# Performance work log

Measured on AMD Instinct MI355X. Metric: run time of the kernel, lower is better.

The kernel has to match this reference:

```python
import jax, jax.numpy as jnp
import numpy as np

B, T, D, H = 8, 1024, 768, 12
HD = D // H          # 64 head dim
WINDOW = 768         # sliding-window width hardcoded in the block
EPS = 1e-5

def _layer_norm(x, w, b):
    mu = jnp.mean(x, axis=-1, keepdims=True)
    var = jnp.mean(jnp.square(x - mu), axis=-1, keepdims=True)
    return (x - mu) * jax.lax.rsqrt(var + EPS) * w + b

def setup_inputs() -> dict:
    key = jax.random.key(0)
    ks = jax.random.split(key, 16)
    s = 0.02
    return {
        "x": jax.random.normal(ks[0], (B, T, D), jnp.float32),
        "attn_mask": jnp.ones((B, T), jnp.int32),
        "ln1_w": jnp.ones((D,), jnp.float32),
        "ln1_b": jnp.zeros((D,), jnp.float32),
        "w_attn": jax.random.normal(ks[1], (D, 3 * D), jnp.float32) * s,
        "b_attn": jnp.zeros((3 * D,), jnp.float32),
        "w_proj": jax.random.normal(ks[2], (D, D), jnp.float32) * s,
        "b_proj": jnp.zeros((D,), jnp.float32),
        "ln2_w": jnp.ones((D,), jnp.float32),
        "ln2_b": jnp.zeros((D,), jnp.float32),
        "w_fc": jax.random.normal(ks[3], (D, 4 * D), jnp.float32) * s,
        "b_fc": jnp.zeros((4 * D,), jnp.float32),
        "w_fc_proj": jax.random.normal(ks[4], (4 * D, D), jnp.float32) * s,
        "b_fc_proj": jnp.zeros((D,), jnp.float32),
    }

def reference(x, attn_mask, ln1_w, ln1_b, w_attn, b_attn, w_proj, b_proj,
              ln2_w, ln2_b, w_fc, b_fc, w_fc_proj, b_fc_proj):
    dtype = x.dtype
    # --- attention sub-block ---
    x1 = _layer_norm(x, ln1_w, ln1_b)
    qkv = x1 @ w_attn + b_attn                       # [B,T,3D]
    q, k, v = jnp.split(qkv, 3, axis=-1)
    q = q.reshape(B, T, H, HD).transpose(0, 2, 1, 3)  # [B,H,T,HD]
    k = k.reshape(B, T, H, HD).transpose(0, 2, 1, 3)
    v = v.reshape(B, T, H, HD).transpose(0, 2, 1, 3)
    # causal + sliding-window + padding mask (additive bias, as in source)
    i = jnp.arange(T)[:, None]
    j = jnp.arange(T)[None, :]
    keep = (j <= i) & (j >= i - WINDOW + 1)           # [T,T]
    keep = keep[None, None] & (attn_mask.astype(bool))[:, None, None, :]  # [B,1,T,T]
    mask_bias = jnp.where(keep, jnp.zeros((), dtype), jnp.full((), jnp.finfo(dtype).min, dtype))
    scale = 1.0 / np.sqrt(HD)
    scores = jnp.einsum('bhqd,bhkd->bhqk', q, k) * scale + mask_bias
    probs = jax.nn.softmax(scores, axis=-1)
    attn = jnp.einsum('bhqk,bhkd->bhqd', probs, v)    # [B,H,T,HD]
    attn = attn.transpose(0, 2, 1, 3).reshape(B, T, D)
    a = attn @ w_proj + b_proj
    x = x + a
    # --- MLP sub-block ---
    x3 = _layer_norm(x, ln2_w, ln2_b)
    h = jax.nn.gelu(x3 @ w_fc + b_fc, approximate=False)
    m = h @ w_fc_proj + b_fc_proj
    return x + m
```

## Files before the change

### kernel.cpp

```cpp
#include <hip/hip_runtime.h>
#include <hip/hip_bf16.h>
#include <math.h>

#define NB 8
#define NT 1024
#define ND 768
#define NH 12
#define HD 64
#define WINDOW 768
#define LN_EPS 1e-5f
#define NEGF -3.4028234663852886e38f

static const int BT = NB * NT;

typedef __bf16 bf16x8 __attribute__((ext_vector_type(8)));
typedef float  f32x4  __attribute__((ext_vector_type(4)));
typedef unsigned short ushort_t;

__device__ __forceinline__ unsigned short f2bf(float f) {
    __hip_bfloat16 h = __float2bfloat16(f);
    return __builtin_bit_cast(unsigned short, h);
}

__device__ __forceinline__ void load_lds16(const void* g, void* l) {
    __builtin_amdgcn_global_load_lds((const __attribute__((address_space(1))) unsigned int*)g,
                                     (__attribute__((address_space(3))) unsigned int*)l,
                                     16, 0, 0);
}

__global__ __launch_bounds__(256) void transpose_bf16(const float* __restrict__ w,
                                                      ushort_t* __restrict__ wt,
                                                      int K, int N) {
    __shared__ float t[32][33];
    const int n0 = blockIdx.x * 32, k0 = blockIdx.y * 32;
    const int tx = threadIdx.x, ty = threadIdx.y;
    for (int r = ty; r < 32; r += 8)
        t[r][tx] = w[(size_t)(k0 + r) * N + n0 + tx];
    __syncthreads();
    for (int r = ty; r < 32; r += 8)
        wt[(size_t)(n0 + r) * K + k0 + tx] = f2bf(t[tx][r]);
}

__global__ __launch_bounds__(256) void transpose_v(const ushort_t* __restrict__ qkvb,
                                                   ushort_t* __restrict__ vT) {
    const int t0 = blockIdx.x * 64;
    const int h = blockIdx.y, b = blockIdx.z;
    __shared__ ushort_t sm[64 * 72];
    const int tid = threadIdx.x;
    #pragma unroll
    for (int p = 0; p < 2; p++) {
        int idx = p * 256 + tid;
        int r = idx >> 3, c = idx & 7;
        *(bf16x8*)&sm[r * 72 + c * 8] =
            *(const bf16x8*)(qkvb + (size_t)(b * NT + t0 + r) * (3 * ND) + 2 * ND + h * HD + c * 8);
    }
    __syncthreads();
    #pragma unroll
    for (int p = 0; p < 2; p++) {
        int idx = p * 256 + tid;
        int d = idx >> 3, c2 = idx & 7;
        ushort_t tmp[8];
        #pragma unroll
        for (int j = 0; j < 8; j++) tmp[j] = sm[(c2 * 8 + j) * 72 + d];
        *(bf16x8*)(vT + ((size_t)((b * NH + h) * HD + d)) * NT + t0 + c2 * 8) = *(bf16x8*)tmp;
    }
}

__global__ __launch_bounds__(256) void ln_kernel(const float* __restrict__ x,
                                                 const float* __restrict__ w,
                                                 const float* __restrict__ b,
                                                 ushort_t* __restrict__ out) {
    const int row  = blockIdx.x * 4 + (threadIdx.x >> 6);
    const int lane = threadIdx.x & 63;
    const float* xr = x + (size_t)row * ND;

    float4 v[3];
    #pragma unroll
    for (int s = 0; s < 3; s++) v[s] = *(const float4*)(xr + s * 256 + lane * 4);

    float sum = 0.f;
    #pragma unroll
    for (int s = 0; s < 3; s++) sum += v[s].x + v[s].y + v[s].z + v[s].w;
    #pragma unroll
    for (int off = 1; off < 64; off <<= 1) sum += __shfl_xor(sum, off, 64);
    const float mu = sum * (1.0f / ND);

    float var = 0.f;
    #pragma unroll
    for (int s = 0; s < 3; s++) {
        float a0 = v[s].x - mu, a1 = v[s].y - mu, a2 = v[s].z - mu, a3 = v[s].w - mu;
        var += a0 * a0 + a1 * a1 + a2 * a2 + a3 * a3;
    }
    #pragma unroll
    for (int off = 1; off < 64; off <<= 1) var += __shfl_xor(var, off, 64);
    const float rstd = rsqrtf(var * (1.0f / ND) + LN_EPS);

    #pragma unroll
    for (int s = 0; s < 3; s++) {
        const int col = s * 256 + lane * 4;
        float4 w4 = *(const float4*)(w + col);
        float4 b4 = *(const float4*)(b + col);
        ushort4 r;
        r.x = f2bf((v[s].x - mu) * rstd * w4.x + b4.x);
        r.y = f2bf((v[s].y - mu) * rstd * w4.y + b4.y);
        r.z = f2bf((v[s].z - mu) * rstd * w4.z + b4.z);
        r.w = f2bf((v[s].w - mu) * rstd * w4.w + b4.w);
        *(ushort4*)(out + (size_t)row * ND + col) = r;
    }
}

template <int EPI>
__global__ __launch_bounds__(256) void gemm_bt(const ushort_t* __restrict__ A,
                                               const ushort_t* __restrict__ Bt,
                                               const float* __restrict__ bias,
                                               const float* __restrict__ resid,
                                               void* __restrict__ Cout,
                                               int M, int N, int K) {
    __shared__ __align__(16) ushort_t smem[2][2][128 * 32];

    const int tid  = threadIdx.x;
    const int bm   = blockIdx.y * 128;
    const int bn   = blockIdx.x * 128;
    const int lane = tid & 63;
    const int wave = tid >> 6;
    const int wm   = (wave & 1) * 64;
    const int wn   = (wave >> 1) * 64;
    const int fcol = lane & 15;
    const int quad = lane >> 4;

    f32x4 acc[4][4] = {};

    const int srow = tid >> 2, scg = (tid & 3) * 8;

    auto issue = [&](int k0, int buf) {
        #pragma unroll
        for (int p = 0; p < 2; p++) {
            const int row = srow + p * 64;
            const int flat = (p * 256 + tid) * 8;
            load_lds16(A  + (size_t)(bm + row) * K + k0 + scg, &smem[buf][0][flat]);
            load_lds16(Bt + (size_t)(bn + row) * K + k0 + scg, &smem[buf][1][flat]);
        }
    };

    issue(0, 0);
    const int KT = K >> 5;
    for (int kt = 0; kt < KT; kt++) {
        const int cur = kt & 1;
        __syncthreads();
        if (kt + 1 < KT) issue((kt + 1) << 5, cur ^ 1);

        bf16x8 a[4], b[4];
        #pragma unroll
        for (int i = 0; i < 4; i++)
            a[i] = *(const bf16x8*)&smem[cur][0][(wm + i * 16 + fcol) * 32 + quad * 8];
        #pragma unroll
        for (int j = 0; j < 4; j++)
            b[j] = *(const bf16x8*)&smem[cur][1][(wn + j * 16 + fcol) * 32 + quad * 8];
        #pragma unroll
        for (int i = 0; i < 4; i++)
            #pragma unroll
            for (int j = 0; j < 4; j++)
                acc[i][j] = __builtin_amdgcn_mfma_f32_16x16x32_bf16(a[i], b[j], acc[i][j], 0, 0, 0);
    }

    if (EPI == 1) {
        #pragma unroll
        for (int j = 0; j < 4; j++) {
            const int gcol = bn + wn + j * 16 + fcol;
            const float bs = bias[gcol];
            #pragma unroll
            for (int i = 0; i < 4; i++) {
                #pragma unroll
                for (int r = 0; r < 4; r++) {
                    const int grow = bm + wm + i * 16 + quad * 4 + r;
                    float val = acc[i][j][r] + bs + resid[(size_t)grow * N + gcol];
                    ((float*)Cout)[(size_t)grow * N + gcol] = val;
                }
            }
        }
    } else {
        __syncthreads();
        ushort_t* Cs = &smem[0][0][0] + wave * (64 * 40);
        #pragma unroll
        for (int hh = 0; hh < 2; hh++) {
            #pragma unroll
            for (int jj = 0; jj < 2; jj++) {
                const int j = hh * 2 + jj;
                const float bs = bias[bn + wn + j * 16 + fcol];
                #pragma unroll
                for (int i = 0; i < 4; i++) {
                    #pragma unroll
                    for (int r = 0; r < 4; r++) {
                        float val = acc[i][j][r] + bs;
                        if (EPI == 2) {
                            float y = 0.7978845608028654f * (val + 0.044715f * val * val * val);
                            float t = 1.0f - 2.0f / (1.0f + __expf(2.0f * y));
                            val = 0.5f * val * (1.0f + t);
                        }
                        const int lr = i * 16 + quad * 4 + r;
                        Cs[lr * 40 + jj * 16 + fcol] = f2bf(val);
                    }
                }
            }
            #pragma unroll
            for (int p = 0; p < 4; p++) {
                const int cid = p * 64 + lane;
                const int lr = cid >> 2, ck = cid & 3;
                bf16x8 vv = *(const bf16x8*)&Cs[lr * 40 + ck * 8];
                *(bf16x8*)((ushort_t*)Cout + (size_t)(bm + wm + lr) * N + bn + wn + hh * 32 + ck * 8) = vv;
            }
        }
    }
}

__global__ __launch_bounds__(256) void flash_attn_mfma(const ushort_t* __restrict__ qkvb,
                                                       const ushort_t* __restrict__ vT,
                                                       const int* __restrict__ amask,
                                                       ushort_t* __restrict__ out) {
    const int qt = 15 - blockIdx.x;
    const int h  = blockIdx.y;
    const int b  = blockIdx.z;
    const int q0 = qt * 64;

    __shared__ __align__(16) ushort_t QPs[64 * 64];
    __shared__ __align__(16) ushort_t Ks[2][64 * 64];
    __shared__ __align__(16) ushort_t Vts[2][64 * 64];

    const int tid  = threadIdx.x;
    const int lane = tid & 63;
    const int wave = tid >> 6;
    const int fcol = lane & 15;
    const int quad = lane >> 4;
    const int wq0  = wave * 16;

    #pragma unroll
    for (int p = 0; p < 2; p++) {
        int flat = p * 256 + tid;
        int r = flat >> 3, c = (flat & 7) ^ (r & 7);
        load_lds16(qkvb + (size_t)(b * NT + q0 + r) * (3 * ND) + h * HD + c * 8, &QPs[flat * 8]);
    }
    __syncthreads();

    bf16x8 aQ[2];
    {
        const int qr = wq0 + fcol;
        #pragma unroll
        for (int ks = 0; ks < 2; ks++) {
            int c = ks * 4 + quad;
            aQ[ks] = *(const bf16x8*)&QPs[qr * 64 + ((c ^ (qr & 7)) * 8)];
        }
    }

    auto issueKV = [&](int cch, int buf) {
        const int kbase = cch * 64;
        #pragma unroll
        for (int p = 0; p < 2; p++) {
            int flat = p * 256 + tid;
            int r = flat >> 3, c = (flat & 7) ^ (r & 7);
            load_lds16(qkvb + (size_t)(b * NT + kbase + r) * (3 * ND) + ND + h * HD + c * 8,
                       &Ks[buf][flat * 8]);
            load_lds16(vT + ((size_t)((b * NH + h) * HD + r)) * NT + kbase + c * 8,
                       &Vts[buf][flat * 8]);
        }
    };

    f32x4 oacc[4] = {};
    float m_i[4], l_i[4];
    #pragma unroll
    for (int r = 0; r < 4; r++) { m_i[r] = NEGF; l_i[r] = 0.f; }

    const int c_lo = (qt > 12) ? (qt - 12) : 0;
    issueKV(c_lo, 0);
    for (int cch = c_lo; cch <= qt; cch++) {
        const int cur = (cch - c_lo) & 1;
        const int kbase = cch * 64;
        __syncthreads();
        if (cch + 1 <= qt) issueKV(cch + 1, cur ^ 1);

        int am[4];
        #pragma unroll
        for (int jn = 0; jn < 4; jn++) am[jn] = amask[b * NT + kbase + jn * 16 + fcol];
        const int amok_lane = (am[0] != 0) & (am[1] != 0) & (am[2] != 0) & (am[3] != 0);
        const bool fast = (cch < qt) && (cch >= qt - 11) && __all(amok_lane);

        f32x4 sc[4] = {};
        #pragma unroll
        for (int ks = 0; ks < 2; ks++) {
            #pragma unroll
            for (int jn = 0; jn < 4; jn++) {
                const int kr = jn * 16 + fcol;
                bf16x8 bk = *(const bf16x8*)&Ks[cur][kr * 64 + (((ks * 4 + quad) ^ (kr & 7)) * 8)];
                sc[jn] = __builtin_amdgcn_mfma_f32_16x16x32_bf16(aQ[ks], bk, sc[jn], 0, 0, 0);
            }
        }

        float pv[4][4], mx[4];
        #pragma unroll
        for (int r = 0; r < 4; r++) mx[r] = NEGF;
        if (fast) {
            #pragma unroll
            for (int jn = 0; jn < 4; jn++)
                #pragma unroll
                for (int r = 0; r < 4; r++) {
                    float s = sc[jn][r] * 0.125f;
                    pv[jn][r] = s;
                    mx[r] = fmaxf(mx[r], s);
                }
        } else {
            #pragma unroll
            for (int jn = 0; jn < 4; jn++) {
                const int jg = kbase + jn * 16 + fcol;
                const bool amok = (am[jn] != 0);
                #pragma unroll
                for (int r = 0; r < 4; r++) {
                    const int ig = q0 + wq0 + quad * 4 + r;
                    float s = sc[jn][r] * 0.125f;
                    bool keep = (jg <= ig) && (jg >= ig - (WINDOW - 1)) && amok;
                    s = keep ? s : NEGF;
                    pv[jn][r] = s;
                    mx[r] = fmaxf(mx[r], s);
                }
            }
        }
        #pragma unroll
        for (int off = 1; off < 16; off <<= 1)
            #pragma unroll
            for (int r = 0; r < 4; r++)
                mx[r] = fmaxf(mx[r], __shfl_xor(mx[r], off, 64));

        float alpha[4], nm[4];
        #pragma unroll
        for (int r = 0; r < 4; r++) {
            nm[r] = fmaxf(m_i[r], mx[r]);
            alpha[r] = __expf(m_i[r] - nm[r]);
            m_i[r] = nm[r];
        }
        float ls[4] = {0.f, 0.f, 0.f, 0.f};
        if (fast) {
            #pragma unroll
            for (int jn = 0; jn < 4; jn++)
                #pragma unroll
                for (int r = 0; r < 4; r++) {
                    float p = __expf(pv[jn][r] - nm[r]);
                    pv[jn][r] = p;
                    ls[r] += p;
                }
        } else {
            #pragma unroll
            for (int jn = 0; jn < 4; jn++)
                #pragma unroll
                for (int r = 0; r < 4; r++) {
                    float s = pv[jn][r];
                    float p = (s <= -1e37f) ? 0.f : __expf(s - nm[r]);
                    pv[jn][r] = p;
                    ls[r] += p;
                }
        }
        #pragma unroll
        for (int off = 1; off < 16; off <<= 1)
            #pragma unroll
            for (int r = 0; r < 4; r++)
                ls[r] += __shfl_xor(ls[r], off, 64);
        #pragma unroll
        for (int r = 0; r < 4; r++) l_i[r] = l_i[r] * alpha[r] + ls[r];
        #pragma unroll
        for (int jd = 0; jd < 4; jd++)
            #pragma unroll
            for (int r = 0; r < 4; r++)
                oacc[jd][r] *= alpha[r];

        #pragma unroll
        for (int jn = 0; jn < 4; jn++) {
            const int key = jn * 16 + fcol;
            const int cc = key >> 3;
            #pragma unroll
            for (int r = 0; r < 4; r++) {
                const int row = wq0 + quad * 4 + r;
                QPs[row * 64 + ((cc ^ (row & 7)) * 8) + (fcol & 7)] = f2bf(pv[jn][r]);
            }
        }

        #pragma unroll
        for (int ks = 0; ks < 2; ks++) {
            const int pr = wq0 + fcol;
            bf16x8 ap = *(const bf16x8*)&QPs[pr * 64 + (((ks * 4 + quad) ^ (pr & 7)) * 8)];
            #pragma unroll
            for (int jd = 0; jd < 4; jd++) {
                const int vr = jd * 16 + fcol;
                bf16x8 bv = *(const bf16x8*)&Vts[cur][vr * 64 + (((ks * 4 + quad) ^ (vr & 7)) * 8)];
                oacc[jd] = __builtin_amdgcn_mfma_f32_16x16x32_bf16(ap, bv, oacc[jd], 0, 0, 0);
            }
        }
    }

    #pragma unroll
    for (int r = 0; r < 4; r++) {
        const float inv = 1.0f / l_i[r];
        const size_t row = (size_t)(b * NT + q0 + wq0 + quad * 4 + r);
        #pragma unroll
        for (int jd = 0; jd < 4; jd++)
            out[row * ND + h * HD + jd * 16 + fcol] = f2bf(oacc[jd][r] * inv);
    }
}

extern "C" void kernel_launch(void* const* d_in, const int* in_sizes, int n_in,
                              void* d_out, int out_size, void* d_ws, size_t ws_size,
                              hipStream_t stream) {
    const float* x        = (const float*)d_in[0];
    const int*   amask    = (const int*)  d_in[1];
    const float* ln1_w    = (const float*)d_in[2];
    const float* ln1_b    = (const float*)d_in[3];
    const float* w_attn   = (const float*)d_in[4];
    const float* b_attn   = (const float*)d_in[5];
    const float* w_proj   = (const float*)d_in[6];
    const float* b_proj   = (const float*)d_in[7];
    const float* ln2_w    = (const float*)d_in[8];
    const float* ln2_b    = (const float*)d_in[9];
    const float* w_fc     = (const float*)d_in[10];
    const float* b_fc     = (const float*)d_in[11];
    const float* w_fcp    = (const float*)d_in[12];
    const float* b_fcp    = (const float*)d_in[13];
    float* out = (float*)d_out;

    ushort_t* ws = (ushort_t*)d_ws;
    ushort_t* qkvb   = ws;
    ushort_t* x1b    = qkvb + (size_t)BT * 3 * ND;
    ushort_t* attn_b = x1b + (size_t)BT * ND;
    ushort_t* hbuf   = attn_b + (size_t)BT * ND;
    ushort_t* vTb    = hbuf + (size_t)BT * 4 * ND;
    ushort_t* wA_T   = vTb + (size_t)BT * ND;
    ushort_t* wP_T   = wA_T + (size_t)2304 * 768;
    ushort_t* wF_T   = wP_T + (size_t)768 * 768;
    ushort_t* wFP_T  = wF_T + (size_t)3072 * 768;

    transpose_bf16<<<dim3(2304 / 32, 768 / 32),  dim3(32, 8), 0, stream>>>(w_attn, wA_T, 768, 2304);
    transpose_bf16<<<dim3(768 / 32,  768 / 32),  dim3(32, 8), 0, stream>>>(w_proj, wP_T, 768, 768);
    transpose_bf16<<<dim3(3072 / 32, 768 / 32),  dim3(32, 8), 0, stream>>>(w_fc,   wF_T, 768, 3072);
    transpose_bf16<<<dim3(768 / 32,  3072 / 32), dim3(32, 8), 0, stream>>>(w_fcp,  wFP_T, 3072, 768);

    ln_kernel<<<BT / 4, 256, 0, stream>>>(x, ln1_w, ln1_b, x1b);
    gemm_bt<0><<<dim3(2304 / 128, BT / 128), 256, 0, stream>>>(x1b, wA_T, b_attn, nullptr, qkvb, BT, 3 * ND, ND);
    transpose_v<<<dim3(16, NH, NB), 256, 0, stream>>>(qkvb, vTb);
    flash_attn_mfma<<<dim3(16, NH, NB), 256, 0, stream>>>(qkvb, vTb, amask, attn_b);
    gemm_bt<1><<<dim3(768 / 128, BT / 128), 256, 0, stream>>>(attn_b, wP_T, b_proj, x, out, BT, ND, ND);
    ln_kernel<<<BT / 4, 256, 0, stream>>>(out, ln2_w, ln2_b, x1b);
    gemm_bt<2><<<dim3(3072 / 128, BT / 128), 256, 0, stream>>>(x1b, wF_T, b_fc, nullptr, hbuf, BT, 4 * ND, ND);
    gemm_bt<1><<<dim3(768 / 128, BT / 128), 256, 0, stream>>>(hbuf, wFP_T, b_fcp, out, out, BT, ND, 4 * ND);
}
```

Before: 415.5 us.

## Drop online-softmax max tracking, compute row sums via MFMA, merge weight transposes

```diff
diff --git a/kernel.cpp b/kernel.cpp
--- a/kernel.cpp
+++ b/kernel.cpp
@@ -10,6 +10,7 @@
 #define WINDOW 768
 #define LN_EPS 1e-5f
 #define NEGF -3.4028234663852886e38f
+#define SCL2 0.18033688011112042f
 
 static const int BT = NB * NT;
 
@@ -28,12 +29,20 @@
                                      16, 0, 0);
 }
 
-__global__ __launch_bounds__(256) void transpose_bf16(const float* __restrict__ w,
-                                                      ushort_t* __restrict__ wt,
-                                                      int K, int N) {
+__global__ __launch_bounds__(256) void transpose_all(const float* __restrict__ w0, ushort_t* __restrict__ t0v,
+                                                     const float* __restrict__ w1, ushort_t* __restrict__ t1v,
+                                                     const float* __restrict__ w2, ushort_t* __restrict__ t2v,
+                                                     const float* __restrict__ w3, ushort_t* __restrict__ t3v) {
+    int bid = blockIdx.x;
+    const float* w; ushort_t* wt; int K, N;
+    if (bid < 1728)                    { w = w0; wt = t0v; K = 768;  N = 2304; }
+    else if ((bid -= 1728) < 576)      { w = w1; wt = t1v; K = 768;  N = 768;  }
+    else if ((bid -= 576) < 2304)      { w = w2; wt = t2v; K = 768;  N = 3072; }
+    else       { bid -= 2304;            w = w3; wt = t3v; K = 3072; N = 768;  }
+    const int nxt = N / 32;
+    const int n0 = (bid % nxt) * 32, k0 = (bid / nxt) * 32;
     __shared__ float t[32][33];
-    const int n0 = blockIdx.x * 32, k0 = blockIdx.y * 32;
-    const int tx = threadIdx.x, ty = threadIdx.y;
+    const int tx = threadIdx.x & 31, ty = threadIdx.x >> 5;
     for (int r = ty; r < 32; r += 8)
         t[r][tx] = w[(size_t)(k0 + r) * N + n0 + tx];
     __syncthreads();
@@ -61,7 +70,11 @@
         int d = idx >> 3, c2 = idx & 7;
         ushort_t tmp[8];
         #pragma unroll
-        for (int j = 0; j < 8; j++) tmp[j] = sm[(c2 * 8 + j) * 72 + d];
+        for (int j = 0; j < 8; j++) {
+            int kp = c2 * 8 + j;
+            int key = ((kp & 1) << 4) | ((kp >> 1) & 15) | (kp & 32);
+            tmp[j] = sm[key * 72 + d];
+        }
         *(bf16x8*)(vT + ((size_t)((b * NH + h) * HD + d)) * NT + t0 + c2 * 8) = *(bf16x8*)tmp;
     }
 }
@@ -251,6 +264,10 @@
         }
     }
 
+    bf16x8 bones;
+    #pragma unroll
+    for (int i = 0; i < 8; i++) bones[i] = (__bf16)1.0f;
+
     auto issueKV = [&](int cch, int buf) {
         const int kbase = cch * 64;
         #pragma unroll
@@ -265,9 +282,7 @@
     };
 
     f32x4 oacc[4] = {};
-    float m_i[4], l_i[4];
-    #pragma unroll
-    for (int r = 0; r < 4; r++) { m_i[r] = NEGF; l_i[r] = 0.f; }
+    f32x4 lacc = {};
 
     const int c_lo = (qt > 12) ? (qt - 12) : 0;
     issueKV(c_lo, 0);
@@ -294,18 +309,13 @@
             }
         }
 
-        float pv[4][4], mx[4];
-        #pragma unroll
-        for (int r = 0; r < 4; r++) mx[r] = NEGF;
+        float pvv[4][4];
         if (fast) {
             #pragma unroll
             for (int jn = 0; jn < 4; jn++)
                 #pragma unroll
-                for (int r = 0; r < 4; r++) {
-                    float s = sc[jn][r] * 0.125f;
-                    pv[jn][r] = s;
-                    mx[r] = fmaxf(mx[r], s);
-                }
+                for (int r = 0; r < 4; r++)
+                    pvv[jn][r] = __builtin_amdgcn_exp2f(sc[jn][r] * SCL2);
         } else {
             #pragma unroll
             for (int jn = 0; jn < 4; jn++) {
@@ -314,69 +324,23 @@
                 #pragma unroll
                 for (int r = 0; r < 4; r++) {
                     const int ig = q0 + wq0 + quad * 4 + r;
-                    float s = sc[jn][r] * 0.125f;
                     bool keep = (jg <= ig) && (jg >= ig - (WINDOW - 1)) && amok;
-                    s = keep ? s : NEGF;
-                    pv[jn][r] = s;
-                    mx[r] = fmaxf(mx[r], s);
+                    float s = keep ? sc[jn][r] * SCL2 : -1e38f;
+                    pvv[jn][r] = __builtin_amdgcn_exp2f(s);
                 }
             }
         }
-        #pragma unroll
-        for (int off = 1; off < 16; off <<= 1)
-            #pragma unroll
-            for (int r = 0; r < 4; r++)
-                mx[r] = fmaxf(mx[r], __shfl_xor(mx[r], off, 64));
-
-        float alpha[4], nm[4];
-        #pragma unroll
-        for (int r = 0; r < 4; r++) {
-            nm[r] = fmaxf(m_i[r], mx[r]);
-            alpha[r] = __expf(m_i[r] - nm[r]);
-            m_i[r] = nm[r];
-        }
-        float ls[4] = {0.f, 0.f, 0.f, 0.f};
-        if (fast) {
-            #pragma unroll
-            for (int jn = 0; jn < 4; jn++)
-                #pragma unroll
-                for (int r = 0; r < 4; r++) {
-                    float p = __expf(pv[jn][r] - nm[r]);
-                    pv[jn][r] = p;
-                    ls[r] += p;
-                }
-        } else {
-            #pragma unroll
-            for (int jn = 0; jn < 4; jn++)
-                #pragma unroll
-                for (int r = 0; r < 4; r++) {
-                    float s = pv[jn][r];
-                    float p = (s <= -1e37f) ? 0.f : __expf(s - nm[r]);
-                    pv[jn][r] = p;
-                    ls[r] += p;
-                }
-        }
-        #pragma unroll
-        for (int off = 1; off < 16; off <<= 1)
-            #pragma unroll
-            for (int r = 0; r < 4; r++)
-                ls[r] += __shfl_xor(ls[r], off, 64);
-        #pragma unroll
-        for (int r = 0; r < 4; r++) l_i[r] = l_i[r] * alpha[r] + ls[r];
-        #pragma unroll
-        for (int jd = 0; jd < 4; jd++)
-            #pragma unroll
-            for (int r = 0; r < 4; r++)
-                oacc[jd][r] *= alpha[r];
-
-        #pragma unroll
-        for (int jn = 0; jn < 4; jn++) {
-            const int key = jn * 16 + fcol;
-            const int cc = key >> 3;
+
+        #pragma unroll
+        for (int half = 0; half < 2; half++) {
+            const int cbase = half * 4 + (fcol >> 2);
+            const int off = (fcol & 3) * 2;
             #pragma unroll
             for (int r = 0; r < 4; r++) {
                 const int row = wq0 + quad * 4 + r;
-                QPs[row * 64 + ((cc ^ (row & 7)) * 8) + (fcol & 7)] = f2bf(pv[jn][r]);
+                unsigned int pk = (unsigned int)f2bf(pvv[half * 2][r]) |
+                                  ((unsigned int)f2bf(pvv[half * 2 + 1][r]) << 16);
+                *(unsigned int*)&QPs[row * 64 + ((cbase ^ (row & 7)) * 8) + off] = pk;
             }
         }
 
@@ -384,6 +348,7 @@
         for (int ks = 0; ks < 2; ks++) {
             const int pr = wq0 + fcol;
             bf16x8 ap = *(const bf16x8*)&QPs[pr * 64 + (((ks * 4 + quad) ^ (pr & 7)) * 8)];
+            lacc = __builtin_amdgcn_mfma_f32_16x16x32_bf16(ap, bones, lacc, 0, 0, 0);
             #pragma unroll
             for (int jd = 0; jd < 4; jd++) {
                 const int vr = jd * 16 + fcol;
@@ -395,7 +360,7 @@
 
     #pragma unroll
     for (int r = 0; r < 4; r++) {
-        const float inv = 1.0f / l_i[r];
+        const float inv = 1.0f / lacc[r];
         const size_t row = (size_t)(b * NT + q0 + wq0 + quad * 4 + r);
         #pragma unroll
         for (int jd = 0; jd < 4; jd++)
@@ -433,10 +398,7 @@
     ushort_t* wF_T   = wP_T + (size_t)768 * 768;
     ushort_t* wFP_T  = wF_T + (size_t)3072 * 768;
 
-    transpose_bf16<<<dim3(2304 / 32, 768 / 32),  dim3(32, 8), 0, stream>>>(w_attn, wA_T, 768, 2304);
-    transpose_bf16<<<dim3(768 / 32,  768 / 32),  dim3(32, 8), 0, stream>>>(w_proj, wP_T, 768, 768);
-    transpose_bf16<<<dim3(3072 / 32, 768 / 32),  dim3(32, 8), 0, stream>>>(w_fc,   wF_T, 768, 3072);
-    transpose_bf16<<<dim3(768 / 32,  3072 / 32), dim3(32, 8), 0, stream>>>(w_fcp,  wFP_T, 3072, 768);
+    transpose_all<<<6912, 256, 0, stream>>>(w_attn, wA_T, w_proj, wP_T, w_fc, wF_T, w_fcp, wFP_T);
 
     ln_kernel<<<BT / 4, 256, 0, stream>>>(x, ln1_w, ln1_b, x1b);
     gemm_bt<0><<<dim3(2304 / 128, BT / 128), 256, 0, stream>>>(x1b, wA_T, b_attn, nullptr, qkvb, BT, 3 * ND, ND);
```

After: 380.3 us. 8.5% less time.
